# Kernel optimization log

Measured on AMD Instinct MI355X. Metric: run time of the kernel, lower is better.

## Reference

```python
import jax, jax.numpy as jnp
import numpy as np

EPS = 1e-5

def layernorm2d(x, w, b):
    # nn.LayerNorm([T, C]): normalize jointly over last two dims, affine shape [T, C]
    mu = jnp.mean(x, axis=(-2, -1), keepdims=True)
    var = jnp.mean(jnp.square(x - mu), axis=(-2, -1), keepdims=True)
    return (x - mu) * jax.lax.rsqrt(var + EPS) * w + b


def setup_inputs() -> dict:
    key = jax.random.key(0)
    ks = jax.random.split(key, 10)
    B, T, C = 64, 512, 512
    s = 0.02
    inputs = jax.random.normal(ks[0], (B, T, C), dtype=jnp.float32)
    ln1_w = jnp.ones((T, C), dtype=jnp.float32)
    ln1_b = jnp.zeros((T, C), dtype=jnp.float32)
    ln2_w = jnp.ones((T, C), dtype=jnp.float32)
    ln2_b = jnp.zeros((T, C), dtype=jnp.float32)
    # TriU: row i holds the Linear(i+1,1) weights for prefix 0..i -> lower-triangular [T,T]
    tri_M = jax.random.normal(ks[1], (T, T), dtype=jnp.float32) * s
    tri_b = jax.random.normal(ks[2], (T,), dtype=jnp.float32) * s
    d1_w = jax.random.normal(ks[3], (C, C), dtype=jnp.float32) * s  # dense_1: out = x @ d1_w.T + d1_b
    d1_b = jax.random.normal(ks[4], (C,), dtype=jnp.float32) * s
    d2_w = jax.random.normal(ks[5], (C, C), dtype=jnp.float32) * s
    d2_b = jax.random.normal(ks[6], (C,), dtype=jnp.float32) * s
    return {"inputs": inputs, "ln1_w": ln1_w, "ln1_b": ln1_b,
            "ln2_w": ln2_w, "ln2_b": ln2_b,
            "tri_M": tri_M, "tri_b": tri_b,
            "d1_w": d1_w, "d1_b": d1_b, "d2_w": d2_w, "d2_b": d2_b}


def reference(inputs, ln1_w, ln1_b, ln2_w, ln2_b, tri_M, tri_b, d1_w, d1_b, d2_w, d2_b):
    # x: [B, T, C]
    x = layernorm2d(inputs, ln1_w, ln1_b)
    # TriU time mixer: out[b,i,c] = sum_{j<=i} M[i,j] * x[b,j,c] + tri_b[i]
    M = jnp.tril(tri_M)
    x = jnp.einsum('it,btc->bic', M, x) + tri_b[None, :, None]
    x = layernorm2d(x + inputs, ln2_w, ln2_b)
    # channel mixer MLP (dropout = 0)
    h = jax.nn.gelu(jnp.einsum('btc,hc->bth', x, d1_w) + d1_b, approximate=False)
    y = jnp.einsum('bth,ch->btc', h, d2_w) + d2_b
    return x + y
```

## Files before the change

kernel.cpp:

```cpp
#include <hip/hip_runtime.h>
#include <hip/hip_bf16.h>
#include <math.h>


#define B_ 64
#define T_ 512
#define C_ 512
#define TC_ (T_ * C_)
static_assert(TC_ == 262144, "");

typedef __attribute__((ext_vector_type(8))) short bf16x8;
typedef __attribute__((ext_vector_type(4))) float f32x4;

__device__ __forceinline__ unsigned short f2bf(float f) {
  union { float f; unsigned u; } v; v.f = f;
  unsigned r = v.u + 0x7FFF + ((v.u >> 16) & 1);
  return (unsigned short)(r >> 16);
}
__device__ __forceinline__ float bf2f(unsigned short h) {
  union { unsigned u; float f; } v; v.u = ((unsigned)h) << 16; return v.f;
}

__device__ __forceinline__ void load16_lds(const void* gsrc, void* ldst) {
  __builtin_amdgcn_global_load_lds(
      (const __attribute__((address_space(1))) unsigned int*)gsrc,
      (__attribute__((address_space(3))) unsigned int*)ldst,
      16, 0, 0);
}

__global__ __launch_bounds__(256) void conv_weights(
    const float* __restrict__ triM, const float* __restrict__ d1w,
    const float* __restrict__ d2w, unsigned short* __restrict__ Mb,
    unsigned short* __restrict__ W1b, unsigned short* __restrict__ W2b) {
  const int idx = blockIdx.x * 256 + threadIdx.x;
  const int i = idx >> 9, j = idx & 511;
  Mb[idx]  = (j <= i) ? f2bf(triM[idx]) : (unsigned short)0;
  W1b[idx] = f2bf(d1w[idx]);
  W2b[idx] = f2bf(d2w[idx]);
}

__global__ __launch_bounds__(256) void ln_stats(const float* __restrict__ x,
                                                float* __restrict__ red) {
  const int b = blockIdx.x;
  const int s = blockIdx.y;
  const float4* p = (const float4*)(x + (size_t)b * TC_) + (size_t)s * 4096;
  float s1 = 0.f, s2 = 0.f;
  for (int i = threadIdx.x; i < 4096; i += 256) {
    float4 v = p[i];
    s1 += v.x + v.y + v.z + v.w;
    s2 += v.x * v.x + v.y * v.y + v.z * v.z + v.w * v.w;
  }
#pragma unroll
  for (int o = 32; o; o >>= 1) { s1 += __shfl_down(s1, o, 64); s2 += __shfl_down(s2, o, 64); }
  __shared__ float sm[8];
  const int w = threadIdx.x >> 6, lane = threadIdx.x & 63;
  if (lane == 0) { sm[w * 2] = s1; sm[w * 2 + 1] = s2; }
  __syncthreads();
  if (threadIdx.x == 0) {
    float a = 0.f, c = 0.f;
    for (int i = 0; i < 4; ++i) { a += sm[2 * i]; c += sm[2 * i + 1]; }
    atomicAdd(&red[b * 2], a);
    atomicAdd(&red[b * 2 + 1], c);
  }
}

__global__ __launch_bounds__(256) void ln1_norm_t(
    const float* __restrict__ x, const float* __restrict__ w,
    const float* __restrict__ bvec, const float* __restrict__ red1,
    unsigned short* __restrict__ XnT) {
  __shared__ unsigned short tile[64][65];
  const int b = blockIdx.z;
  const int t0 = blockIdx.y * 64;
  const int c0 = blockIdx.x * 64;
  const float mu = red1[b * 2] * (1.f / TC_);
  const float rstd = rsqrtf(red1[b * 2 + 1] * (1.f / TC_) - mu * mu + 1e-5f);
  const int tid = threadIdx.x;
  const int r = tid >> 4;
  const int cg = (tid & 15) * 4;
#pragma unroll
  for (int rr = 0; rr < 4; ++rr) {
    const int t = t0 + rr * 16 + r;
    const float4 xv = *(const float4*)&x[((size_t)b * T_ + t) * C_ + c0 + cg];
    const float4 wv = *(const float4*)&w[(size_t)t * C_ + c0 + cg];
    const float4 bv = *(const float4*)&bvec[(size_t)t * C_ + c0 + cg];
    tile[rr * 16 + r][cg + 0] = f2bf((xv.x - mu) * rstd * wv.x + bv.x);
    tile[rr * 16 + r][cg + 1] = f2bf((xv.y - mu) * rstd * wv.y + bv.y);
    tile[rr * 16 + r][cg + 2] = f2bf((xv.z - mu) * rstd * wv.z + bv.z);
    tile[rr * 16 + r][cg + 3] = f2bf((xv.w - mu) * rstd * wv.w + bv.w);
  }
  __syncthreads();
  const int cl = tid >> 2;
  const int tg = (tid & 3) * 16;
  alignas(16) unsigned short tmp[16];
#pragma unroll
  for (int j = 0; j < 16; ++j) tmp[j] = tile[tg + j][cl];
  unsigned short* o = &XnT[((size_t)b * C_ + c0 + cl) * T_ + t0 + tg];
  *(uint4*)&o[0] = *(const uint4*)&tmp[0];
  *(uint4*)&o[8] = *(const uint4*)&tmp[8];
}

__device__ __forceinline__ void gemm_mainloop(
    const unsigned short* __restrict__ Ag,
    const unsigned short* __restrict__ Bg,
    int lda, int ldb, int ktiles,
    unsigned short* Atile, unsigned short* Btile, f32x4 acc[4][4], int tid) {
  const int lane = tid & 63;
  const int w = tid >> 6;
  const int wr = (w >> 1) * 64;
  const int wc = (w & 1) * 64;
  const int m16 = lane & 15;
  const int quad = lane >> 4;
  for (int kt = 0; kt < ktiles; ++kt) {
    const int k0 = kt * 32;
#pragma unroll
    for (int i = 0; i < 2; ++i) {
      const int c = tid + 256 * i;
      const int row = c >> 2, ko = (c & 3) * 8;
      load16_lds(Ag + (size_t)row * lda + k0 + ko, Atile + c * 8);
      load16_lds(Bg + (size_t)row * ldb + k0 + ko, Btile + c * 8);
    }
    __syncthreads();
    bf16x8 af[4], bfr[4];
#pragma unroll
    for (int r = 0; r < 4; ++r)
      af[r] = *(const bf16x8*)&Atile[(wr + r * 16 + m16) * 32 + quad * 8];
#pragma unroll
    for (int c = 0; c < 4; ++c)
      bfr[c] = *(const bf16x8*)&Btile[(wc + c * 16 + m16) * 32 + quad * 8];
#pragma unroll
    for (int r = 0; r < 4; ++r)
#pragma unroll
      for (int c = 0; c < 4; ++c)
        acc[r][c] = __builtin_amdgcn_mfma_f32_16x16x32_bf16(af[r], bfr[c], acc[r][c], 0, 0, 0);
    __syncthreads();
  }
}

__global__ __launch_bounds__(256) void gemm_mixer(
    const unsigned short* __restrict__ Mb, const unsigned short* __restrict__ XnT,
    const float* __restrict__ trib, const float* __restrict__ inp,
    unsigned short* __restrict__ Z, float* __restrict__ red2) {
  __shared__ __align__(16) unsigned short Atile[4096], Btile[4096];
  const int b = blockIdx.z;
  const int i0 = blockIdx.y * 128;
  const int c0 = blockIdx.x * 128;
  f32x4 acc[4][4];
#pragma unroll
  for (int r = 0; r < 4; ++r)
#pragma unroll
    for (int c = 0; c < 4; ++c) acc[r][c] = (f32x4){0.f, 0.f, 0.f, 0.f};
  gemm_mainloop(Mb + (size_t)i0 * T_, XnT + (size_t)b * TC_ + (size_t)c0 * T_,
                T_, T_, (i0 >> 5) + 4, Atile, Btile, acc, threadIdx.x);
  const int tid = threadIdx.x, lane = tid & 63, w = tid >> 6;
  const int wr = (w >> 1) * 64, wc = (w & 1) * 64, m16 = lane & 15, quad = lane >> 4;
  float s1 = 0.f, s2 = 0.f;
#pragma unroll
  for (int r = 0; r < 4; ++r) {
#pragma unroll
    for (int g = 0; g < 4; ++g) {
      const int i = i0 + wr + r * 16 + quad * 4 + g;
      const float tb = trib[i];
      const float* inrow = &inp[((size_t)b * T_ + i) * C_];
      unsigned short* zrow = &Z[((size_t)b * T_ + i) * C_];
#pragma unroll
      for (int c = 0; c < 4; ++c) {
        const int ch = c0 + wc + c * 16 + m16;
        const float v = acc[r][c][g] + tb + inrow[ch];
        zrow[ch] = f2bf(v);
        s1 += v; s2 += v * v;
      }
    }
  }
#pragma unroll
  for (int o = 32; o; o >>= 1) { s1 += __shfl_down(s1, o, 64); s2 += __shfl_down(s2, o, 64); }
  __shared__ float sm[8];
  if (lane == 0) { sm[w * 2] = s1; sm[w * 2 + 1] = s2; }
  __syncthreads();
  if (tid == 0) {
    float a = 0.f, c2 = 0.f;
    for (int i = 0; i < 4; ++i) { a += sm[2 * i]; c2 += sm[2 * i + 1]; }
    atomicAdd(&red2[b * 2], a);
    atomicAdd(&red2[b * 2 + 1], c2);
  }
}

__global__ __launch_bounds__(256) void ln2_norm(
    const unsigned short* __restrict__ Z, const float* __restrict__ red2,
    const float* __restrict__ w, const float* __restrict__ bvec,
    unsigned short* __restrict__ X2) {
  const size_t e = ((size_t)blockIdx.x * 256 + threadIdx.x) * 8;
  const int b = (int)(e >> 18);
  const int tc = (int)(e & (TC_ - 1));
  const float mu = red2[b * 2] * (1.f / TC_);
  const float rstd = rsqrtf(red2[b * 2 + 1] * (1.f / TC_) - mu * mu + 1e-5f);
  uint4 zp = *(const uint4*)&Z[e];
  const unsigned short* zs = (const unsigned short*)&zp;
  alignas(16) float wv[8], bb[8];
  *(float4*)&wv[0] = *(const float4*)&w[tc];
  *(float4*)&wv[4] = *(const float4*)&w[tc + 4];
  *(float4*)&bb[0] = *(const float4*)&bvec[tc];
  *(float4*)&bb[4] = *(const float4*)&bvec[tc + 4];
  alignas(16) unsigned short o[8];
#pragma unroll
  for (int j = 0; j < 8; ++j)
    o[j] = f2bf((bf2f(zs[j]) - mu) * rstd * wv[j] + bb[j]);
  *(uint4*)&X2[e] = *(const uint4*)&o[0];
}

__global__ __launch_bounds__(256) void gemm_d1(
    const unsigned short* __restrict__ X2, const unsigned short* __restrict__ W1b,
    const float* __restrict__ d1b, unsigned short* __restrict__ H) {
  __shared__ __align__(16) unsigned short Atile[4096], Btile[4096];
  const int i0 = blockIdx.y * 128;
  const int n0 = blockIdx.x * 128;
  f32x4 acc[4][4];
#pragma unroll
  for (int r = 0; r < 4; ++r)
#pragma unroll
    for (int c = 0; c < 4; ++c) acc[r][c] = (f32x4){0.f, 0.f, 0.f, 0.f};
  gemm_mainloop(X2 + (size_t)i0 * C_, W1b + (size_t)n0 * C_, C_, C_, 16,
                Atile, Btile, acc, threadIdx.x);
  const int tid = threadIdx.x, lane = tid & 63, w = tid >> 6;
  const int wr = (w >> 1) * 64, wc = (w & 1) * 64, m16 = lane & 15, quad = lane >> 4;
#pragma unroll
  for (int r = 0; r < 4; ++r) {
#pragma unroll
    for (int g = 0; g < 4; ++g) {
      const int row = i0 + wr + r * 16 + quad * 4 + g;
#pragma unroll
      for (int c = 0; c < 4; ++c) {
        const int n = n0 + wc + c * 16 + m16;
        const float v = acc[r][c][g] + d1b[n];
        const float gl = 0.5f * v * (1.0f + erff(v * 0.70710678118654752f));
        H[(size_t)row * C_ + n] = f2bf(gl);
      }
    }
  }
}

__global__ __launch_bounds__(256) void gemm_d2(
    const unsigned short* __restrict__ H, const unsigned short* __restrict__ W2b,
    const float* __restrict__ d2b, const unsigned short* __restrict__ X2,
    float* __restrict__ out) {
  __shared__ __align__(16) unsigned short Atile[4096], Btile[4096];
  const int i0 = blockIdx.y * 128;
  const int n0 = blockIdx.x * 128;
  f32x4 acc[4][4];
#pragma unroll
  for (int r = 0; r < 4; ++r)
#pragma unroll
    for (int c = 0; c < 4; ++c) acc[r][c] = (f32x4){0.f, 0.f, 0.f, 0.f};
  gemm_mainloop(H + (size_t)i0 * C_, W2b + (size_t)n0 * C_, C_, C_, 16,
                Atile, Btile, acc, threadIdx.x);
  const int tid = threadIdx.x, lane = tid & 63, w = tid >> 6;
  const int wr = (w >> 1) * 64, wc = (w & 1) * 64, m16 = lane & 15, quad = lane >> 4;
#pragma unroll
  for (int r = 0; r < 4; ++r) {
#pragma unroll
    for (int g = 0; g < 4; ++g) {
      const int row = i0 + wr + r * 16 + quad * 4 + g;
#pragma unroll
      for (int c = 0; c < 4; ++c) {
        const int n = n0 + wc + c * 16 + m16;
        out[(size_t)row * C_ + n] = acc[r][c][g] + d2b[n] + bf2f(X2[(size_t)row * C_ + n]);
      }
    }
  }
}

extern "C" void kernel_launch(void* const* d_in, const int* in_sizes, int n_in,
                              void* d_out, int out_size, void* d_ws, size_t ws_size,
                              hipStream_t stream) {
  const float* inp  = (const float*)d_in[0];
  const float* ln1w = (const float*)d_in[1];
  const float* ln1b = (const float*)d_in[2];
  const float* ln2w = (const float*)d_in[3];
  const float* ln2b = (const float*)d_in[4];
  const float* triM = (const float*)d_in[5];
  const float* trib = (const float*)d_in[6];
  const float* d1w  = (const float*)d_in[7];
  const float* d1b  = (const float*)d_in[8];
  const float* d2w  = (const float*)d_in[9];
  const float* d2b  = (const float*)d_in[10];
  float* out = (float*)d_out;

  char* ws = (char*)d_ws;
  float* red1 = (float*)ws;
  float* red2 = (float*)(ws + 512);
  unsigned short* Mb  = (unsigned short*)(ws + 1024);
  unsigned short* W1b = Mb + TC_;
  unsigned short* W2b = W1b + TC_;
  unsigned short* XnT = W2b + TC_;
  unsigned short* Z   = XnT + (size_t)B_ * TC_;
  unsigned short* X2  = Z + (size_t)B_ * TC_;
  unsigned short* H   = X2 + (size_t)B_ * TC_;

  hipMemsetAsync(ws, 0, 1024, stream);
  conv_weights<<<1024, 256, 0, stream>>>(triM, d1w, d2w, Mb, W1b, W2b);
  ln_stats<<<dim3(B_, 16), 256, 0, stream>>>(inp, red1);
  ln1_norm_t<<<dim3(8, 8, B_), 256, 0, stream>>>(inp, ln1w, ln1b, red1, XnT);
  gemm_mixer<<<dim3(4, 4, B_), 256, 0, stream>>>(Mb, XnT, trib, inp, Z, red2);
  ln2_norm<<<8192, 256, 0, stream>>>(Z, red2, ln2w, ln2b, X2);
  gemm_d1<<<dim3(4, 256), 256, 0, stream>>>(X2, W1b, d1b, H);
  gemm_d2<<<dim3(4, 256), 256, 0, stream>>>(H, W2b, d2b, X2, out);
}
```

Baseline: 275.6 us.

## Double-buffer GEMM LDS tiles, XOR-swizzle LDS layout, and XCD-aware block remap

The shared GEMM mainloop now prefetches the next K tile into a second LDS buffer while MFMAs run on the current one, removing one barrier per iteration. It also XOR-swizzles the 16-byte chunk offset within each LDS row to cut bank conflicts on the fragment reads. Blocks are remapped so that consecutive tiles land on the same XCD, which should improve L2 reuse. LDS use per block doubles, which may lower occupancy. The prefetch uses global_load_lds issued before the compute, so correctness depends on the barrier placement covering those asynchronous writes.

```diff
diff --git a/kernel.cpp b/kernel.cpp
--- a/kernel.cpp
+++ b/kernel.cpp
@@ -99,51 +99,72 @@
   *(uint4*)&o[8] = *(const uint4*)&tmp[8];
 }
 
+__device__ __forceinline__ void stage_tiles(
+    const unsigned short* __restrict__ Ag, const unsigned short* __restrict__ Bg,
+    int lda, int ldb, int k0, unsigned short* Abuf, unsigned short* Bbuf, int tid) {
+#pragma unroll
+  for (int i = 0; i < 2; ++i) {
+    const int c = tid + 256 * i;
+    const int row = c >> 2;
+    const int ko = (((c & 3) ^ ((row >> 1) & 3)) * 8);
+    load16_lds(Ag + (size_t)row * lda + k0 + ko, Abuf + c * 8);
+    load16_lds(Bg + (size_t)row * ldb + k0 + ko, Bbuf + c * 8);
+  }
+}
+
 __device__ __forceinline__ void gemm_mainloop(
     const unsigned short* __restrict__ Ag,
     const unsigned short* __restrict__ Bg,
     int lda, int ldb, int ktiles,
-    unsigned short* Atile, unsigned short* Btile, f32x4 acc[4][4], int tid) {
+    unsigned short* Atile, unsigned short* Btile,
+    f32x4 acc[4][4], int tid) {
   const int lane = tid & 63;
   const int w = tid >> 6;
   const int wr = (w >> 1) * 64;
   const int wc = (w & 1) * 64;
   const int m16 = lane & 15;
   const int quad = lane >> 4;
+  const int ps = (quad ^ ((m16 >> 1) & 3)) * 8;
+  unsigned short* Acur = Atile;        unsigned short* Bcur = Btile;
+  unsigned short* Anxt = Atile + 4096; unsigned short* Bnxt = Btile + 4096;
+  stage_tiles(Ag, Bg, lda, ldb, 0, Acur, Bcur, tid);
+  __syncthreads();
   for (int kt = 0; kt < ktiles; ++kt) {
-    const int k0 = kt * 32;
-#pragma unroll
-    for (int i = 0; i < 2; ++i) {
-      const int c = tid + 256 * i;
-      const int row = c >> 2, ko = (c & 3) * 8;
-      load16_lds(Ag + (size_t)row * lda + k0 + ko, Atile + c * 8);
-      load16_lds(Bg + (size_t)row * ldb + k0 + ko, Btile + c * 8);
-    }
-    __syncthreads();
+    if (kt + 1 < ktiles)
+      stage_tiles(Ag, Bg, lda, ldb, (kt + 1) * 32, Anxt, Bnxt, tid);
     bf16x8 af[4], bfr[4];
 #pragma unroll
     for (int r = 0; r < 4; ++r)
-      af[r] = *(const bf16x8*)&Atile[(wr + r * 16 + m16) * 32 + quad * 8];
+      af[r] = *(const bf16x8*)&Acur[(wr + r * 16 + m16) * 32 + ps];
 #pragma unroll
     for (int c = 0; c < 4; ++c)
-      bfr[c] = *(const bf16x8*)&Btile[(wc + c * 16 + m16) * 32 + quad * 8];
+      bfr[c] = *(const bf16x8*)&Bcur[(wc + c * 16 + m16) * 32 + ps];
 #pragma unroll
     for (int r = 0; r < 4; ++r)
 #pragma unroll
       for (int c = 0; c < 4; ++c)
         acc[r][c] = __builtin_amdgcn_mfma_f32_16x16x32_bf16(af[r], bfr[c], acc[r][c], 0, 0, 0);
     __syncthreads();
-  }
+    unsigned short* t;
+    t = Acur; Acur = Anxt; Anxt = t;
+    t = Bcur; Bcur = Bnxt; Bnxt = t;
+  }
+}
+
+__device__ __forceinline__ int xcd_swizzle_1024(int bid) {
+  return (bid & 7) * 128 + (bid >> 3);
 }
 
 __global__ __launch_bounds__(256) void gemm_mixer(
     const unsigned short* __restrict__ Mb, const unsigned short* __restrict__ XnT,
     const float* __restrict__ trib, const float* __restrict__ inp,
     unsigned short* __restrict__ Z, float* __restrict__ red2) {
-  __shared__ __align__(16) unsigned short Atile[4096], Btile[4096];
-  const int b = blockIdx.z;
-  const int i0 = blockIdx.y * 128;
-  const int c0 = blockIdx.x * 128;
+  __shared__ __align__(16) unsigned short Atile[8192], Btile[8192];
+  const int bid = (blockIdx.z * 4 + blockIdx.y) * 4 + blockIdx.x;
+  const int swz = xcd_swizzle_1024(bid);
+  const int b = swz >> 4;
+  const int i0 = ((swz >> 2) & 3) * 128;
+  const int c0 = (swz & 3) * 128;
   f32x4 acc[4][4];
 #pragma unroll
   for (int r = 0; r < 4; ++r)
@@ -210,9 +231,11 @@
 __global__ __launch_bounds__(256) void gemm_d1(
     const unsigned short* __restrict__ X2, const unsigned short* __restrict__ W1b,
     const float* __restrict__ d1b, unsigned short* __restrict__ H) {
-  __shared__ __align__(16) unsigned short Atile[4096], Btile[4096];
-  const int i0 = blockIdx.y * 128;
-  const int n0 = blockIdx.x * 128;
+  __shared__ __align__(16) unsigned short Atile[8192], Btile[8192];
+  const int bid = blockIdx.y * 4 + blockIdx.x;
+  const int swz = xcd_swizzle_1024(bid);
+  const int i0 = (swz >> 2) * 128;
+  const int n0 = (swz & 3) * 128;
   f32x4 acc[4][4];
 #pragma unroll
   for (int r = 0; r < 4; ++r)
@@ -242,9 +265,11 @@
     const unsigned short* __restrict__ H, const unsigned short* __restrict__ W2b,
     const float* __restrict__ d2b, const unsigned short* __restrict__ X2,
     float* __restrict__ out) {
-  __shared__ __align__(16) unsigned short Atile[4096], Btile[4096];
-  const int i0 = blockIdx.y * 128;
-  const int n0 = blockIdx.x * 128;
+  __shared__ __align__(16) unsigned short Atile[8192], Btile[8192];
+  const int bid = blockIdx.y * 4 + blockIdx.x;
+  const int swz = xcd_swizzle_1024(bid);
+  const int i0 = (swz >> 2) * 128;
+  const int n0 = (swz & 3) * 128;
   f32x4 acc[4][4];
 #pragma unroll
   for (int r = 0; r < 4; ++r)
```

Result: faster. 266.6 us (-3.3%).

## Use 256x256 double-buffered swizzled-LDS GEMM tiles with XCD block remapping

Applied to the files above, without the earlier changes.

Replaces the 128x128 single-buffered GEMM mainloop with a 256x256 tile over 8 waves and two LDS buffers, so global-to-LDS loads for the next k-tile overlap MFMA work. It adds an XOR swizzle on LDS chunk placement to reduce bank conflicts, raises MFMA wave priority, and remaps block ids across XCDs. The three GEMM kernels now launch 256 blocks of 512 threads, cutting redundant operand reloads. The risks are one-wave grids with poor load balance, especially for the triangular mixer, and higher register pressure.

```diff
diff --git a/kernel.cpp b/kernel.cpp
--- a/kernel.cpp
+++ b/kernel.cpp
@@ -99,73 +99,107 @@
   *(uint4*)&o[8] = *(const uint4*)&tmp[8];
 }
 
-__device__ __forceinline__ void gemm_mainloop(
-    const unsigned short* __restrict__ Ag,
-    const unsigned short* __restrict__ Bg,
-    int lda, int ldb, int ktiles,
-    unsigned short* Atile, unsigned short* Btile, f32x4 acc[4][4], int tid) {
-  const int lane = tid & 63;
-  const int w = tid >> 6;
-  const int wr = (w >> 1) * 64;
-  const int wc = (w & 1) * 64;
-  const int m16 = lane & 15;
-  const int quad = lane >> 4;
-  for (int kt = 0; kt < ktiles; ++kt) {
-    const int k0 = kt * 32;
-#pragma unroll
-    for (int i = 0; i < 2; ++i) {
-      const int c = tid + 256 * i;
-      const int row = c >> 2, ko = (c & 3) * 8;
-      load16_lds(Ag + (size_t)row * lda + k0 + ko, Atile + c * 8);
-      load16_lds(Bg + (size_t)row * ldb + k0 + ko, Btile + c * 8);
-    }
+__device__ __forceinline__ void stage_tile256(
+    const unsigned short* __restrict__ Ag, const unsigned short* __restrict__ Bg,
+    int k0, unsigned short* As, unsigned short* Bs, int tid) {
+#pragma unroll
+  for (int j = 0; j < 2; ++j) {
+    const int c = tid + 512 * j;
+    const int row = c >> 2;
+    const int l = (c & 3) ^ ((row ^ (row >> 2)) & 3);
+    load16_lds(Ag + ((size_t)row << 9) + k0 + l * 8, As + c * 8);
+  }
+#pragma unroll
+  for (int j = 0; j < 2; ++j) {
+    const int c = tid + 512 * j;
+    const int row = c >> 2;
+    const int l = (c & 3) ^ ((row ^ (row >> 2)) & 3);
+    load16_lds(Bg + ((size_t)row << 9) + k0 + l * 8, Bs + c * 8);
+  }
+}
+
+__device__ __forceinline__ void mfma_tile(
+    const unsigned short* __restrict__ Ac, const unsigned short* __restrict__ Bc,
+    int arow, int brow, int co, f32x4 acc[8][4]) {
+  bf16x8 af[8], bfr[4];
+#pragma unroll
+  for (int m = 0; m < 8; ++m)
+    af[m] = *(const bf16x8*)&Ac[arow + m * 512 + co];
+#pragma unroll
+  for (int n = 0; n < 4; ++n)
+    bfr[n] = *(const bf16x8*)&Bc[brow + n * 512 + co];
+  __builtin_amdgcn_s_setprio(1);
+#pragma unroll
+  for (int m = 0; m < 8; ++m)
+#pragma unroll
+    for (int n = 0; n < 4; ++n)
+      acc[m][n] = __builtin_amdgcn_mfma_f32_16x16x32_bf16(af[m], bfr[n], acc[m][n], 0, 0, 0);
+  __builtin_amdgcn_s_setprio(0);
+}
+
+__device__ __forceinline__ void gemm_mainloop256(
+    const unsigned short* __restrict__ Ag, const unsigned short* __restrict__ Bg,
+    int ktiles,
+    unsigned short* lds, f32x4 acc[8][4], int tid) {
+  const int lane = tid & 63, w = tid >> 6;
+  const int wm = w >> 2, wn = w & 3;
+  const int m16 = lane & 15, quad = lane >> 4;
+  unsigned short* A0 = lds;
+  unsigned short* B0 = lds + 8192;
+  unsigned short* A1 = lds + 16384;
+  unsigned short* B1 = lds + 24576;
+  const int arow = (wm * 128 + m16) * 32;
+  const int brow = (wn * 64 + m16) * 32;
+  const int co = ((quad ^ ((m16 ^ (m16 >> 2)) & 3)) * 8);
+  stage_tile256(Ag, Bg, 0, A0, B0, tid);
+  __syncthreads();
+  for (int kt = 0; kt < ktiles; kt += 2) {
+    stage_tile256(Ag, Bg, (kt + 1) * 32, A1, B1, tid);
+    mfma_tile(A0, B0, arow, brow, co, acc);
     __syncthreads();
-    bf16x8 af[4], bfr[4];
-#pragma unroll
-    for (int r = 0; r < 4; ++r)
-      af[r] = *(const bf16x8*)&Atile[(wr + r * 16 + m16) * 32 + quad * 8];
-#pragma unroll
-    for (int c = 0; c < 4; ++c)
-      bfr[c] = *(const bf16x8*)&Btile[(wc + c * 16 + m16) * 32 + quad * 8];
-#pragma unroll
-    for (int r = 0; r < 4; ++r)
-#pragma unroll
-      for (int c = 0; c < 4; ++c)
-        acc[r][c] = __builtin_amdgcn_mfma_f32_16x16x32_bf16(af[r], bfr[c], acc[r][c], 0, 0, 0);
+    if (kt + 2 < ktiles)
+      stage_tile256(Ag, Bg, (kt + 2) * 32, A0, B0, tid);
+    mfma_tile(A1, B1, arow, brow, co, acc);
     __syncthreads();
   }
 }
 
-__global__ __launch_bounds__(256) void gemm_mixer(
+__device__ __forceinline__ int xcd_swizzle_256(int bid) {
+  return ((bid & 7) << 5) | (bid >> 3);
+}
+
+__global__ __launch_bounds__(512, 2) void gemm_mixer(
     const unsigned short* __restrict__ Mb, const unsigned short* __restrict__ XnT,
     const float* __restrict__ trib, const float* __restrict__ inp,
     unsigned short* __restrict__ Z, float* __restrict__ red2) {
-  __shared__ __align__(16) unsigned short Atile[4096], Btile[4096];
-  const int b = blockIdx.z;
-  const int i0 = blockIdx.y * 128;
-  const int c0 = blockIdx.x * 128;
-  f32x4 acc[4][4];
-#pragma unroll
-  for (int r = 0; r < 4; ++r)
-#pragma unroll
-    for (int c = 0; c < 4; ++c) acc[r][c] = (f32x4){0.f, 0.f, 0.f, 0.f};
-  gemm_mainloop(Mb + (size_t)i0 * T_, XnT + (size_t)b * TC_ + (size_t)c0 * T_,
-                T_, T_, (i0 >> 5) + 4, Atile, Btile, acc, threadIdx.x);
+  __shared__ __align__(16) unsigned short lds[32768];
+  const int swz = xcd_swizzle_256((int)blockIdx.x);
+  const int b = swz >> 2;
+  const int i0 = ((swz >> 1) & 1) * 256;
+  const int c0 = (swz & 1) * 256;
+  f32x4 acc[8][4];
+#pragma unroll
+  for (int m = 0; m < 8; ++m)
+#pragma unroll
+    for (int n = 0; n < 4; ++n) acc[m][n] = (f32x4){0.f, 0.f, 0.f, 0.f};
+  gemm_mainloop256(Mb + (size_t)i0 * T_, XnT + (size_t)b * TC_ + (size_t)c0 * T_,
+                   (i0 + 256) >> 5, lds, acc, (int)threadIdx.x);
   const int tid = threadIdx.x, lane = tid & 63, w = tid >> 6;
-  const int wr = (w >> 1) * 64, wc = (w & 1) * 64, m16 = lane & 15, quad = lane >> 4;
+  const int wm = w >> 2, wn = w & 3, m16 = lane & 15, quad = lane >> 4;
+  const int rbase = i0 + wm * 128, cbase = c0 + wn * 64;
   float s1 = 0.f, s2 = 0.f;
 #pragma unroll
-  for (int r = 0; r < 4; ++r) {
+  for (int m = 0; m < 8; ++m) {
 #pragma unroll
     for (int g = 0; g < 4; ++g) {
-      const int i = i0 + wr + r * 16 + quad * 4 + g;
+      const int i = rbase + m * 16 + quad * 4 + g;
       const float tb = trib[i];
       const float* inrow = &inp[((size_t)b * T_ + i) * C_];
       unsigned short* zrow = &Z[((size_t)b * T_ + i) * C_];
 #pragma unroll
-      for (int c = 0; c < 4; ++c) {
-        const int ch = c0 + wc + c * 16 + m16;
-        const float v = acc[r][c][g] + tb + inrow[ch];
+      for (int n = 0; n < 4; ++n) {
+        const int ch = cbase + n * 16 + m16;
+        const float v = acc[m][n][g] + tb + inrow[ch];
         zrow[ch] = f2bf(v);
         s1 += v; s2 += v * v;
       }
@@ -173,12 +207,12 @@
   }
 #pragma unroll
   for (int o = 32; o; o >>= 1) { s1 += __shfl_down(s1, o, 64); s2 += __shfl_down(s2, o, 64); }
-  __shared__ float sm[8];
-  if (lane == 0) { sm[w * 2] = s1; sm[w * 2 + 1] = s2; }
+  float* smf = (float*)lds;
+  if (lane == 0) { smf[w * 2] = s1; smf[w * 2 + 1] = s2; }
   __syncthreads();
   if (tid == 0) {
     float a = 0.f, c2 = 0.f;
-    for (int i = 0; i < 4; ++i) { a += sm[2 * i]; c2 += sm[2 * i + 1]; }
+    for (int i = 0; i < 8; ++i) { a += smf[2 * i]; c2 += smf[2 * i + 1]; }
     atomicAdd(&red2[b * 2], a);
     atomicAdd(&red2[b * 2 + 1], c2);
   }
@@ -207,62 +241,67 @@
   *(uint4*)&X2[e] = *(const uint4*)&o[0];
 }
 
-__global__ __launch_bounds__(256) void gemm_d1(
+__global__ __launch_bounds__(512, 2) void gemm_d1(
     const unsigned short* __restrict__ X2, const unsigned short* __restrict__ W1b,
     const float* __restrict__ d1b, unsigned short* __restrict__ H) {
-  __shared__ __align__(16) unsigned short Atile[4096], Btile[4096];
-  const int i0 = blockIdx.y * 128;
-  const int n0 = blockIdx.x * 128;
-  f32x4 acc[4][4];
-#pragma unroll
-  for (int r = 0; r < 4; ++r)
-#pragma unroll
-    for (int c = 0; c < 4; ++c) acc[r][c] = (f32x4){0.f, 0.f, 0.f, 0.f};
-  gemm_mainloop(X2 + (size_t)i0 * C_, W1b + (size_t)n0 * C_, C_, C_, 16,
-                Atile, Btile, acc, threadIdx.x);
+  __shared__ __align__(16) unsigned short lds[32768];
+  const int swz = xcd_swizzle_256((int)blockIdx.x);
+  const int n0 = (swz >> 7) * 256;
+  const int i0 = (swz & 127) * 256;
+  f32x4 acc[8][4];
+#pragma unroll
+  for (int m = 0; m < 8; ++m)
+#pragma unroll
+    for (int n = 0; n < 4; ++n) acc[m][n] = (f32x4){0.f, 0.f, 0.f, 0.f};
+  gemm_mainloop256(X2 + (size_t)i0 * C_, W1b + (size_t)n0 * C_, 16, lds, acc,
+                   (int)threadIdx.x);
   const int tid = threadIdx.x, lane = tid & 63, w = tid >> 6;
-  const int wr = (w >> 1) * 64, wc = (w & 1) * 64, m16 = lane & 15, quad = lane >> 4;
-#pragma unroll
-  for (int r = 0; r < 4; ++r) {
+  const int wm = w >> 2, wn = w & 3, m16 = lane & 15, quad = lane >> 4;
+  const int rbase = i0 + wm * 128, cbase = n0 + wn * 64;
+#pragma unroll
+  for (int m = 0; m < 8; ++m) {
 #pragma unroll
     for (int g = 0; g < 4; ++g) {
-      const int row = i0 + wr + r * 16 + quad * 4 + g;
-#pragma unroll
-      for (int c = 0; c < 4; ++c) {
-        const int n = n0 + wc + c * 16 + m16;
-        const float v = acc[r][c][g] + d1b[n];
+      const int row = rbase + m * 16 + quad * 4 + g;
+#pragma unroll
+      for (int n = 0; n < 4; ++n) {
+        const int col = cbase + n * 16 + m16;
+        const float v = acc[m][n][g] + d1b[col];
         const float gl = 0.5f * v * (1.0f + erff(v * 0.70710678118654752f));
-        H[(size_t)row * C_ + n] = f2bf(gl);
+        H[(size_t)row * C_ + col] = f2bf(gl);
       }
     }
   }
 }
 
-__global__ __launch_bounds__(256) void gemm_d2(
+__global__ __launch_bounds__(512, 2) void gemm_d2(
     const unsigned short* __restrict__ H, const unsigned short* __restrict__ W2b,
     const float* __restrict__ d2b, const unsigned short* __restrict__ X2,
     float* __restrict__ out) {
-  __shared__ __align__(16) unsigned short Atile[4096], Btile[4096];
-  const int i0 = blockIdx.y * 128;
-  const int n0 = blockIdx.x * 128;
-  f32x4 acc[4][4];
-#pragma unroll
-  for (int r = 0; r < 4; ++r)
-#pragma unroll
-    for (int c = 0; c < 4; ++c) acc[r][c] = (f32x4){0.f, 0.f, 0.f, 0.f};
-  gemm_mainloop(H + (size_t)i0 * C_, W2b + (size_t)n0 * C_, C_, C_, 16,
-                Atile, Btile, acc, threadIdx.x);
+  __shared__ __align__(16) unsigned short lds[32768];
+  const int swz = xcd_swizzle_256((int)blockIdx.x);
+  const int n0 = (swz >> 7) * 256;
+  const int i0 = (swz & 127) * 256;
+  f32x4 acc[8][4];
+#pragma unroll
+  for (int m = 0; m < 8; ++m)
+#pragma unroll
+    for (int n = 0; n < 4; ++n) acc[m][n] = (f32x4){0.f, 0.f, 0.f, 0.f};
+  gemm_mainloop256(H + (size_t)i0 * C_, W2b + (size_t)n0 * C_, 16, lds, acc,
+                   (int)threadIdx.x);
   const int tid = threadIdx.x, lane = tid & 63, w = tid >> 6;
-  const int wr = (w >> 1) * 64, wc = (w & 1) * 64, m16 = lane & 15, quad = lane >> 4;
-#pragma unroll
-  for (int r = 0; r < 4; ++r) {
+  const int wm = w >> 2, wn = w & 3, m16 = lane & 15, quad = lane >> 4;
+  const int rbase = i0 + wm * 128, cbase = n0 + wn * 64;
+#pragma unroll
+  for (int m = 0; m < 8; ++m) {
 #pragma unroll
     for (int g = 0; g < 4; ++g) {
-      const int row = i0 + wr + r * 16 + quad * 4 + g;
-#pragma unroll
-      for (int c = 0; c < 4; ++c) {
-        const int n = n0 + wc + c * 16 + m16;
-        out[(size_t)row * C_ + n] = acc[r][c][g] + d2b[n] + bf2f(X2[(size_t)row * C_ + n]);
+      const int row = rbase + m * 16 + quad * 4 + g;
+#pragma unroll
+      for (int n = 0; n < 4; ++n) {
+        const int col = cbase + n * 16 + m16;
+        out[(size_t)row * C_ + col] =
+            acc[m][n][g] + d2b[col] + bf2f(X2[(size_t)row * C_ + col]);
       }
     }
   }
@@ -299,8 +338,8 @@
   conv_weights<<<1024, 256, 0, stream>>>(triM, d1w, d2w, Mb, W1b, W2b);
   ln_stats<<<dim3(B_, 16), 256, 0, stream>>>(inp, red1);
   ln1_norm_t<<<dim3(8, 8, B_), 256, 0, stream>>>(inp, ln1w, ln1b, red1, XnT);
-  gemm_mixer<<<dim3(4, 4, B_), 256, 0, stream>>>(Mb, XnT, trib, inp, Z, red2);
+  gemm_mixer<<<256, 512, 0, stream>>>(Mb, XnT, trib, inp, Z, red2);
   ln2_norm<<<8192, 256, 0, stream>>>(Z, red2, ln2w, ln2b, X2);
-  gemm_d1<<<dim3(4, 256), 256, 0, stream>>>(X2, W1b, d1b, H);
-  gemm_d2<<<dim3(4, 256), 256, 0, stream>>>(H, W2b, d2b, X2, out);
-}
+  gemm_d1<<<256, 512, 0, stream>>>(X2, W1b, d1b, H);
+  gemm_d2<<<256, 512, 0, stream>>>(H, W2b, d2b, X2, out);
+}
```

Measured after the change: 270.8 us. About the same (-1.8%).
